# Kernel optimization log

Hardware: AMD Instinct MI355X
Metric: run time of the kernel (lower is better)

## Reference

```python
import jax, jax.numpy as jnp
import numpy as np

B, N, E = 8, 2000, 32000
LAT, STY, NF = 128, 64, 10
HEADS, HID = 4, 128
OUT = 3 + NF  # 13
EPS = 1e-5
SLOPE = 0.2


def _lin(k, fi, fo):
    return jax.random.normal(k, (fi, fo), dtype=jnp.float32) / np.sqrt(fi)


def setup_inputs() -> dict:
    key = jax.random.key(0)
    ks = jax.random.split(key, 32)
    inp = {
        'z': jax.random.normal(ks[0], (B, LAT), dtype=jnp.float32),
        'template_x': jax.random.normal(ks[1], (N, NF), dtype=jnp.float32),
        'template_edge_index': jax.random.randint(ks[2], (2, E), 0, N, dtype=jnp.int32),
        # style MLP
        'mlp_w1': _lin(ks[3], LAT, 256), 'mlp_b1': jnp.zeros((256,), jnp.float32),
        'mlp_w2': _lin(ks[4], 256, 512), 'mlp_b2': jnp.zeros((512,), jnp.float32),
        'mlp_w3': _lin(ks[5], 512, STY), 'mlp_b3': jnp.zeros((STY,), jnp.float32),
        # GAT1: in = NF + STY = 74 -> heads*HID = 512, concat
        'gat1_w': _lin(ks[6], NF + STY, HEADS * HID),
        'gat1_as': jax.random.normal(ks[7], (HEADS, HID), jnp.float32) * 0.1,
        'gat1_ad': jax.random.normal(ks[8], (HEADS, HID), jnp.float32) * 0.1,
        'gat1_b': jnp.zeros((HEADS * HID,), jnp.float32),
        'ln1_g': jnp.ones((HEADS * HID,), jnp.float32), 'ln1_b': jnp.zeros((HEADS * HID,), jnp.float32),
        # GAT2: 512 -> 512, concat
        'gat2_w': _lin(ks[9], HEADS * HID, HEADS * HID),
        'gat2_as': jax.random.normal(ks[10], (HEADS, HID), jnp.float32) * 0.1,
        'gat2_ad': jax.random.normal(ks[11], (HEADS, HID), jnp.float32) * 0.1,
        'gat2_b': jnp.zeros((HEADS * HID,), jnp.float32),
        'ln2_g': jnp.ones((HEADS * HID,), jnp.float32), 'ln2_b': jnp.zeros((HEADS * HID,), jnp.float32),
        # GAT3: 512 -> 13, 1 head, no concat
        'gat3_w': _lin(ks[12], HEADS * HID, OUT),
        'gat3_as': jax.random.normal(ks[13], (1, OUT), jnp.float32) * 0.1,
        'gat3_ad': jax.random.normal(ks[14], (1, OUT), jnp.float32) * 0.1,
        'gat3_b': jnp.zeros((OUT,), jnp.float32),
    }
    return inp


def gat_conv(x, src, dst, n_nodes, W, a_src, a_dst, bias, heads, out_ch, concat):
    # x: [NT, F_in]; per-head linear transform
    h = (x @ W).reshape(-1, heads, out_ch)              # [NT, H, C]
    als = jnp.sum(h * a_src[None], axis=-1)             # [NT, H]
    ald = jnp.sum(h * a_dst[None], axis=-1)             # [NT, H]
    logits = jax.nn.leaky_relu(als[src] + ald[dst], SLOPE)   # [E, H]
    # segment softmax over destination nodes (self-loops guarantee nonempty segments)
    mx = jax.ops.segment_max(logits, dst, num_segments=n_nodes)
    alpha = jnp.exp(logits - mx[dst])
    den = jax.ops.segment_sum(alpha, dst, num_segments=n_nodes)
    alpha = alpha / den[dst]                             # [E, H]
    msgs = h[src] * alpha[:, :, None]                    # [E, H, C]
    out = jax.ops.segment_sum(msgs, dst, num_segments=n_nodes)  # [NT, H, C]
    if concat:
        return out.reshape(n_nodes, heads * out_ch) + bias
    return out.mean(axis=1) + bias


def layer_norm(x, g, b):
    mu = jnp.mean(x, axis=-1, keepdims=True)
    var = jnp.mean((x - mu) ** 2, axis=-1, keepdims=True)
    return (x - mu) * jax.lax.rsqrt(var + EPS) * g + b


def reference(z, template_x, template_edge_index,
              mlp_w1, mlp_b1, mlp_w2, mlp_b2, mlp_w3, mlp_b3,
              gat1_w, gat1_as, gat1_ad, gat1_b, ln1_g, ln1_b,
              gat2_w, gat2_as, gat2_ad, gat2_b, ln2_g, ln2_b,
              gat3_w, gat3_as, gat3_ad, gat3_b):
    bsz = z.shape[0]
    n = template_x.shape[0]
    nt = bsz * n
    # batch the template graph: replicate nodes, offset edge indices per graph
    x = jnp.tile(template_x, (bsz, 1))                                  # [NT, NF]
    off = (jnp.arange(bsz, dtype=template_edge_index.dtype) * n)
    ei = (template_edge_index[:, None, :] + off[None, :, None]).reshape(2, -1)  # [2, B*E]
    loops = jnp.arange(nt, dtype=ei.dtype)
    src = jnp.concatenate([ei[0], loops])
    dst = jnp.concatenate([ei[1], loops])
    # style MLP
    s = jax.nn.leaky_relu(z @ mlp_w1 + mlp_b1, SLOPE)
    s = jax.nn.leaky_relu(s @ mlp_w2 + mlp_b2, SLOPE)
    s = s @ mlp_w3 + mlp_b3                                             # [B, STY]
    s_exp = jnp.repeat(s, n, axis=0)                                    # [NT, STY]
    H0 = jnp.concatenate([x, s_exp], axis=1)
    H1 = jax.nn.leaky_relu(gat_conv(H0, src, dst, nt, gat1_w, gat1_as, gat1_ad, gat1_b, HEADS, HID, True), SLOPE)
    H1n = layer_norm(H1, ln1_g, ln1_b)
    H2 = jax.nn.leaky_relu(gat_conv(H1n, src, dst, nt, gat2_w, gat2_as, gat2_ad, gat2_b, HEADS, HID, True), SLOPE)
    H2 = H2 + H1n
    H2n = layer_norm(H2, ln2_g, ln2_b)
    H_out = gat_conv(H2n, src, dst, nt, gat3_w, gat3_as, gat3_ad, gat3_b, 1, OUT, False)  # [NT, 13]
    delta_p = H_out[:, :3]
    delta_f = H_out[:, 3:]
    p_gen = x[:, :3] + delta_p
    X_gen = jnp.concatenate([p_gen, x[:, 3:] + delta_f[:, 3:]], axis=1)  # X[:, :3] overwritten by p_gen
    EF = p_gen[ei[1]] - p_gen[ei[0]]                                     # edge displacement vectors [B*E, 3]
    return X_gen, p_gen, EF
```

## Files before the change

kernel.cpp:

```cpp
#include <hip/hip_runtime.h>
#include <hip/hip_fp16.h>

constexpr int Bz = 8, Nn = 2000, Ee = 32000, NTOT = 16000;
constexpr int XG_OFF = 0, PG_OFF = 160000, EF_OFF = 208000;
#define SLOPE 0.2f
#define EPSL 1e-5f

typedef __attribute__((ext_vector_type(8))) _Float16 f16x8;
typedef __attribute__((ext_vector_type(4))) float float4v;

__device__ __forceinline__ float lrelu(float x) { return x > 0.f ? x : SLOPE * x; }

__device__ __forceinline__ unsigned short f2h(float x) {
  _Float16 hh = (_Float16)x;
  return *(unsigned short*)&hh;
}

__device__ __forceinline__ float wave_max(float v) {
  for (int o = 32; o; o >>= 1) v = fmaxf(v, __shfl_xor(v, o));
  return v;
}
__device__ __forceinline__ float wave_sum(float v) {
  for (int o = 32; o; o >>= 1) v += __shfl_xor(v, o);
  return v;
}

__global__ void hist_k(const int* __restrict__ tei, int* __restrict__ counts) {
  int j = blockIdx.x * 256 + threadIdx.x;
  if (j < Ee) atomicAdd(&counts[tei[Ee + j]], 1);
}

__global__ void scan_k(const int* __restrict__ counts, int* __restrict__ offs) {
  __shared__ int part[256];
  int t = threadIdx.x;
  int loc[8];
  int s = 0;
  for (int i = 0; i < 8; i++) {
    int idx = t * 8 + i;
    int c = (idx < Nn) ? counts[idx] : 0;
    loc[i] = s; s += c;
  }
  part[t] = s;
  __syncthreads();
  for (int o = 1; o < 256; o <<= 1) {
    int v = (t >= o) ? part[t - o] : 0;
    __syncthreads();
    part[t] += v;
    __syncthreads();
  }
  int excl = (t == 0) ? 0 : part[t - 1];
  for (int i = 0; i < 8; i++) {
    int idx = t * 8 + i;
    if (idx < Nn) offs[idx] = excl + loc[i];
  }
  if (t == 255) offs[Nn] = part[255];
}

__global__ void place_k(const int* __restrict__ tei, const int* __restrict__ offs,
                        int* __restrict__ cursor, int* __restrict__ colb) {
  int j = blockIdx.x * 256 + threadIdx.x;
  if (j < Ee) {
    int d = tei[Ee + j];
    int slot = offs[d] + atomicAdd(&cursor[d], 1);
    colb[slot] = tei[j];
  }
}

template <int K, int ACT>
__global__ __launch_bounds__(256) void lin_k(const float* __restrict__ x, const float* __restrict__ w,
                                             const float* __restrict__ bias, float* __restrict__ y,
                                             int O) {
  int gw = blockIdx.x * 4 + (threadIdx.x >> 6);
  int lane = threadIdx.x & 63;
  int bb = gw / O, o = gw - bb * O;
  float acc = 0.f;
#pragma unroll
  for (int k = lane; k < K; k += 64) acc += x[bb * K + k] * w[k * O + o];
  acc = wave_sum(acc);
  if (lane == 0) {
    if (bias) acc += bias[o];
    y[gw] = ACT ? lrelu(acc) : acc;
  }
}

__global__ __launch_bounds__(256) void w2bf_k(const float* __restrict__ W, unsigned short* __restrict__ Bt) {
  __shared__ float tile[32][33];
  int tx = threadIdx.x & 31, ty = threadIdx.x >> 5;
  int x0 = blockIdx.x * 32;
  int y0 = blockIdx.y * 32;
  for (int r = ty; r < 32; r += 8) tile[r][tx] = W[(y0 + r) * 512 + x0 + tx];
  __syncthreads();
  for (int r = ty; r < 32; r += 8) Bt[(x0 + r) * 512 + (y0 + tx)] = f2h(tile[tx][r]);
}

__global__ void w3t_k(const float* __restrict__ W, unsigned short* __restrict__ W3t) {
  for (int idx = threadIdx.x; idx < 8192; idx += 256) {
    int col = idx >> 9, k = idx & 511;
    float v = (col < 13) ? W[k * 13 + col] : 0.f;
    W3t[idx] = f2h(v);
  }
}

__global__ __launch_bounds__(256) void h1_k(const float* __restrict__ tx, const float* __restrict__ g1w,
                                            const float* __restrict__ pb,
                                            const float* __restrict__ a_s, const float* __restrict__ a_d,
                                            unsigned short* __restrict__ h1, float* __restrict__ als,
                                            float* __restrict__ ald) {
  int blk = blockIdx.x;
  int b = blk & 7, nl = blk >> 3;
  int n = b * Nn + nl;
  int head = threadIdx.x >> 6, lane = threadIdx.x & 63;
  int c = head * 128 + 2 * lane;
  float t0 = 0.f, t1 = 0.f;
#pragma unroll
  for (int k = 0; k < 10; k++) {
    float xv = tx[nl * 10 + k];
    float2 wv = *(const float2*)&g1w[k * 512 + c];
    t0 += xv * wv.x; t1 += xv * wv.y;
  }
  float2 pv = *(const float2*)&pb[b * 512 + c];
  float hx = t0 + pv.x, hy = t1 + pv.y;
  ushort2 st; st.x = f2h(hx); st.y = f2h(hy);
  *(ushort2*)&h1[(size_t)n * 512 + c] = st;
  float2 av = *(const float2*)&a_s[c];
  float2 dv = *(const float2*)&a_d[c];
  float pa = wave_sum(hx * av.x + hy * av.y);
  float pd = wave_sum(hx * dv.x + hy * dv.y);
  if (lane == 0) { als[n * 4 + head] = pa; ald[n * 4 + head] = pd; }
}

template <int RESID>
__global__ __launch_bounds__(256) void agg_k(const unsigned short* __restrict__ h,
                                             const float* __restrict__ als, const float* __restrict__ ald,
                                             const float* __restrict__ bias,
                                             const float* __restrict__ g, const float* __restrict__ beta,
                                             const unsigned short* __restrict__ resid,
                                             unsigned short* __restrict__ out,
                                             const int* __restrict__ offs, const int* __restrict__ colb) {
  int blk = blockIdx.x;
  int b = blk & 7, nl = blk >> 3;
  int n = b * Nn + nl;
  int w = threadIdx.x >> 6, lane = threadIdx.x & 63;
  int rs = offs[nl];
  int nit = offs[nl + 1] - rs + 1;
  float aldn = ald[n * 4 + w];

  __shared__ unsigned int alpha_u[4][68];
  __shared__ int sgn[64];
  __shared__ float part[4][512];
  __shared__ float invs[4];
  __shared__ float red[8];
  __shared__ float bcs[2];

  __half2 acc2[4];
#pragma unroll
  for (int j = 0; j < 4; j++) acc2[j] = __float2half2_rn(0.f);

  const unsigned short* hbase = h + lane * 8;
  int hd = lane >> 4;

  if (nit <= 64) {
    int sg = n;
    float logit = -3e38f;
    if (lane < nit) {
      sg = (lane < nit - 1) ? colb[rs + lane] + b * Nn : n;
      logit = lrelu(als[sg * 4 + w] + aldn);
      if (w == 0) sgn[lane] = sg;
    }
    float m = wave_max(logit);
    float raw = (lane < nit) ? __expf(logit - m) : 0.f;
    float den = wave_sum(raw);
    if (lane == 0) invs[w] = 1.f / den;
    __half2 a2 = __float2half2_rn(raw);
    alpha_u[w][lane] = *(unsigned int*)&a2;
    __syncthreads();
    int e = w;
    for (; e + 4 < nit; e += 8) {
      unsigned int au0 = alpha_u[hd][e];
      int sg0 = sgn[e];
      unsigned int au1 = alpha_u[hd][e + 4];
      int sg1 = sgn[e + 4];
      uint4 hv0 = *(const uint4*)(hbase + (size_t)sg0 * 512);
      uint4 hv1 = *(const uint4*)(hbase + (size_t)sg1 * 512);
      __half2 a0 = *(__half2*)&au0;
      __half2 a1 = *(__half2*)&au1;
      acc2[0] = __hfma2(a0, *(__half2*)&hv0.x, acc2[0]);
      acc2[1] = __hfma2(a0, *(__half2*)&hv0.y, acc2[1]);
      acc2[2] = __hfma2(a0, *(__half2*)&hv0.z, acc2[2]);
      acc2[3] = __hfma2(a0, *(__half2*)&hv0.w, acc2[3]);
      acc2[0] = __hfma2(a1, *(__half2*)&hv1.x, acc2[0]);
      acc2[1] = __hfma2(a1, *(__half2*)&hv1.y, acc2[1]);
      acc2[2] = __hfma2(a1, *(__half2*)&hv1.z, acc2[2]);
      acc2[3] = __hfma2(a1, *(__half2*)&hv1.w, acc2[3]);
    }
    if (e < nit) {
      unsigned int au0 = alpha_u[hd][e];
      int sg0 = sgn[e];
      uint4 hv0 = *(const uint4*)(hbase + (size_t)sg0 * 512);
      __half2 a0 = *(__half2*)&au0;
      acc2[0] = __hfma2(a0, *(__half2*)&hv0.x, acc2[0]);
      acc2[1] = __hfma2(a0, *(__half2*)&hv0.y, acc2[1]);
      acc2[2] = __hfma2(a0, *(__half2*)&hv0.z, acc2[2]);
      acc2[3] = __hfma2(a0, *(__half2*)&hv0.w, acc2[3]);
    }
  } else {
    float m = -3e38f;
    for (int i = lane; i < nit; i += 64) {
      int sg = (i < nit - 1) ? colb[rs + i] + b * Nn : n;
      m = fmaxf(m, lrelu(als[sg * 4 + w] + aldn));
    }
    m = wave_max(m);
    float den = 0.f;
    for (int base = 0; base < nit; base += 64) {
      int cnt = min(64, nit - base);
      int sg = n;
      float raw = 0.f;
      if (lane < cnt) {
        int i = base + lane;
        sg = (i < nit - 1) ? colb[rs + i] + b * Nn : n;
        raw = __expf(lrelu(als[sg * 4 + w] + aldn) - m);
        if (w == 0) sgn[lane] = sg;
      }
      den += raw;
      __half2 a2 = __float2half2_rn(raw);
      alpha_u[w][lane] = *(unsigned int*)&a2;
      __syncthreads();
      for (int e = w; e < cnt; e += 4) {
        unsigned int au = alpha_u[hd][e];
        int sge = sgn[e];
        uint4 hv = *(const uint4*)(hbase + (size_t)sge * 512);
        __half2 a2e = *(__half2*)&au;
        acc2[0] = __hfma2(a2e, *(__half2*)&hv.x, acc2[0]);
        acc2[1] = __hfma2(a2e, *(__half2*)&hv.y, acc2[1]);
        acc2[2] = __hfma2(a2e, *(__half2*)&hv.z, acc2[2]);
        acc2[3] = __hfma2(a2e, *(__half2*)&hv.w, acc2[3]);
      }
      __syncthreads();
    }
    den = wave_sum(den);
    if (lane == 0) invs[w] = 1.f / den;
  }

  float fv[8];
#pragma unroll
  for (int j = 0; j < 4; j++) {
    float2 f2 = __half22float2(acc2[j]);
    fv[2 * j] = f2.x; fv[2 * j + 1] = f2.y;
  }
  *(float4*)&part[w][lane * 8] = make_float4(fv[0], fv[1], fv[2], fv[3]);
  *(float4*)&part[w][lane * 8 + 4] = make_float4(fv[4], fv[5], fv[6], fv[7]);
  __syncthreads();

  int c = 2 * (int)threadIdx.x;
  float inv = invs[c >> 7];
  float s0 = part[0][c] + part[1][c] + part[2][c] + part[3][c];
  float s1 = part[0][c + 1] + part[1][c + 1] + part[2][c + 1] + part[3][c + 1];
  float v0 = lrelu(s0 * inv + bias[c]);
  float v1 = lrelu(s1 * inv + bias[c + 1]);
  if (RESID) {
    unsigned int rv = *(const unsigned int*)&resid[(size_t)n * 512 + c];
    __half2 rh = *(__half2*)&rv;
    float2 rf = __half22float2(rh);
    v0 += rf.x; v1 += rf.y;
  }
  float p1 = wave_sum(v0 + v1);
  float p2 = wave_sum(v0 * v0 + v1 * v1);
  if (lane == 0) { red[w] = p1; red[4 + w] = p2; }
  __syncthreads();
  if (threadIdx.x == 0) {
    float s1r = red[0] + red[1] + red[2] + red[3];
    float s2r = red[4] + red[5] + red[6] + red[7];
    float mu = s1r * (1.f / 512.f);
    float var = s2r * (1.f / 512.f) - mu * mu;
    bcs[0] = mu;
    bcs[1] = rsqrtf(var + EPSL);
  }
  __syncthreads();
  float mu = bcs[0], rstd = bcs[1];
  float o0 = (v0 - mu) * rstd * g[c] + beta[c];
  float o1 = (v1 - mu) * rstd * g[c + 1] + beta[c + 1];
  ushort2 st; st.x = f2h(o0); st.y = f2h(o1);
  *(ushort2*)&out[(size_t)n * 512 + c] = st;
}

__global__ __launch_bounds__(256) void gemm2_k(const unsigned short* __restrict__ A,
                                               const unsigned short* __restrict__ Bt,
                                               unsigned short* __restrict__ C,
                                               const float* __restrict__ As, const float* __restrict__ Ad,
                                               float* __restrict__ als2, float* __restrict__ ald2) {
  __shared__ char smem[24576];
  char* sAc = smem;
  char* sBc = smem + 8192;
  int t = threadIdx.x;
  int lane = t & 63, w = t >> 6;
  int wr = w >> 1, wc = w & 1;
  int m0 = blockIdx.y * 64, n0 = blockIdx.x * 128;
  int head = blockIdx.x;

  float4v acc[2][4];
#pragma unroll
  for (int i = 0; i < 2; i++)
#pragma unroll
    for (int j = 0; j < 4; j++) acc[i][j] = (float4v){0.f, 0.f, 0.f, 0.f};

  int sarow[2], saklin[2], sasw[2];
#pragma unroll
  for (int i = 0; i < 2; i++) {
    int slot = i * 256 + t;
    sarow[i] = slot >> 3;
    saklin[i] = (slot & 7) * 16;
    sasw[i] = sarow[i] * 128 + (saklin[i] ^ ((sarow[i] & 7) << 4));
  }
  int sbrow[4], sbklin[4], sbsw[4];
#pragma unroll
  for (int i = 0; i < 4; i++) {
    int slot = i * 256 + t;
    sbrow[i] = slot >> 3;
    sbklin[i] = (slot & 7) * 16;
    sbsw[i] = sbrow[i] * 128 + (sbklin[i] ^ ((sbrow[i] & 7) << 4));
  }

  uint4 va[2], vb[4];
#pragma unroll
  for (int i = 0; i < 2; i++)
    va[i] = *(const uint4*)((const char*)A + (size_t)(m0 + sarow[i]) * 1024 + saklin[i]);
#pragma unroll
  for (int i = 0; i < 4; i++)
    vb[i] = *(const uint4*)((const char*)Bt + (size_t)(n0 + sbrow[i]) * 1024 + sbklin[i]);

  int r_a = wr * 32 + (lane & 15);
  int r_b = wc * 64 + (lane & 15);
  int kbb = (lane >> 4) * 16;
  int sw_a = (r_a & 7) << 4;
  int sw_b = (r_b & 7) << 4;

  for (int k0 = 0; k0 < 512; k0 += 64) {
    if (k0) __syncthreads();
#pragma unroll
    for (int i = 0; i < 2; i++) *(uint4*)(sAc + sasw[i]) = va[i];
#pragma unroll
    for (int i = 0; i < 4; i++) *(uint4*)(sBc + sbsw[i]) = vb[i];
    __syncthreads();
    if (k0 + 64 < 512) {
#pragma unroll
      for (int i = 0; i < 2; i++)
        va[i] = *(const uint4*)((const char*)A + (size_t)(m0 + sarow[i]) * 1024 + (k0 + 64) * 2 + saklin[i]);
#pragma unroll
      for (int i = 0; i < 4; i++)
        vb[i] = *(const uint4*)((const char*)Bt + (size_t)(n0 + sbrow[i]) * 1024 + (k0 + 64) * 2 + sbklin[i]);
    }
#pragma unroll
    for (int ksub = 0; ksub < 2; ksub++) {
      f16x8 af[2], bg[4];
#pragma unroll
      for (int m = 0; m < 2; m++)
        af[m] = *(const f16x8*)(sAc + (r_a + m * 16) * 128 + ((ksub * 64 + kbb) ^ sw_a));
#pragma unroll
      for (int nn = 0; nn < 4; nn++)
        bg[nn] = *(const f16x8*)(sBc + (r_b + nn * 16) * 128 + ((ksub * 64 + kbb) ^ sw_b));
#pragma unroll
      for (int m = 0; m < 2; m++)
#pragma unroll
        for (int nn = 0; nn < 4; nn++)
          acc[m][nn] = __builtin_amdgcn_mfma_f32_16x16x32_f16(af[m], bg[nn], acc[m][nn], 0, 0, 0);
    }
  }

  __syncthreads();
  unsigned short* sC = (unsigned short*)smem;
  int rbase = wr * 32 + (lane >> 4) * 4;
  int cbase = wc * 64 + (lane & 15);
#pragma unroll
  for (int m = 0; m < 2; m++)
#pragma unroll
    for (int nn = 0; nn < 4; nn++)
#pragma unroll
      for (int r = 0; r < 4; r++)
        sC[(rbase + m * 16 + r) * 136 + cbase + nn * 16] = f2h(acc[m][nn][r]);
  __syncthreads();
#pragma unroll
  for (int p = 0; p < 4; p++) {
    int row = p * 16 + (t >> 4);
    int co = (t & 15) * 8;
    uint4 v = *(const uint4*)&sC[row * 136 + co];
    *(uint4*)&C[(size_t)(m0 + row) * 512 + n0 + co] = v;
  }

  __syncthreads();
  float* sRed = (float*)smem;
  int cidx0 = wc * 64 + (lane & 15);
  float asv[4], adv[4];
#pragma unroll
  for (int nn = 0; nn < 4; nn++) {
    asv[nn] = As[head * 128 + cidx0 + nn * 16];
    adv[nn] = Ad[head * 128 + cidx0 + nn * 16];
  }
#pragma unroll
  for (int m = 0; m < 2; m++) {
#pragma unroll
    for (int r = 0; r < 4; r++) {
      float pa = 0.f, pd = 0.f;
#pragma unroll
      for (int nn = 0; nn < 4; nn++) { pa += acc[m][nn][r] * asv[nn]; pd += acc[m][nn][r] * adv[nn]; }
      for (int o = 1; o < 16; o <<= 1) { pa += __shfl_xor(pa, o); pd += __shfl_xor(pd, o); }
      if ((lane & 15) == 0) {
        int rblk = wr * 32 + (lane >> 4) * 4 + m * 16 + r;
        sRed[rblk * 2 + wc] = pa;
        sRed[128 + rblk * 2 + wc] = pd;
      }
    }
  }
  __syncthreads();
  if (t < 64) {
    als2[(m0 + t) * 4 + head] = sRed[t * 2] + sRed[t * 2 + 1];
  } else if (t < 128) {
    int r2 = t - 64;
    ald2[(m0 + r2) * 4 + head] = sRed[128 + r2 * 2] + sRed[128 + r2 * 2 + 1];
  }
}

__global__ __launch_bounds__(256) void gemm3_k(const unsigned short* __restrict__ H,
                                               const unsigned short* __restrict__ W3t,
                                               const float* __restrict__ as3, const float* __restrict__ ad3,
                                               float* __restrict__ h3, float* __restrict__ als3,
                                               float* __restrict__ ald3) {
  int w = threadIdx.x >> 6, l = threadIdx.x & 63;
  int m0 = blockIdx.x * 64 + w * 16;
  int r16 = l & 15, g4 = l >> 4;
  float4v acc = (float4v){0.f, 0.f, 0.f, 0.f};
  const unsigned short* ha = H + (size_t)(m0 + r16) * 512 + g4 * 8;
  const unsigned short* wb = W3t + (size_t)r16 * 512 + g4 * 8;
#pragma unroll
  for (int kk = 0; kk < 16; kk++) {
    f16x8 a = *(const f16x8*)(ha + kk * 32);
    f16x8 bfr = *(const f16x8*)(wb + kk * 32);
    acc = __builtin_amdgcn_mfma_f32_16x16x32_f16(a, bfr, acc, 0, 0, 0);
  }
  int col = r16;
  float asv = (col < 13) ? as3[col] : 0.f;
  float adv = (col < 13) ? ad3[col] : 0.f;
#pragma unroll
  for (int r = 0; r < 4; r++) {
    float v = acc[r];
    int row = m0 + g4 * 4 + r;
    if (col < 13) h3[row * 13 + col] = v;
    float sa = v * asv, sd = v * adv;
    for (int o = 1; o < 16; o <<= 1) { sa += __shfl_xor(sa, o); sd += __shfl_xor(sd, o); }
    if (col == 0) { als3[row] = sa; ald3[row] = sd; }
  }
}

__global__ __launch_bounds__(64) void agg3_k(const float* __restrict__ h3, const float* __restrict__ als3,
                                             const float* __restrict__ ald3, const float* __restrict__ b3,
                                             const float* __restrict__ tx, const int* __restrict__ offs,
                                             const int* __restrict__ colb, float* __restrict__ dout) {
  int blk = blockIdx.x, lane = threadIdx.x;
  int b = blk & 7, nl = blk >> 3;
  int n = b * Nn + nl;
  int rs = offs[nl], deg = offs[nl + 1] - rs;
  float aldn = ald3[n];
  float sl = lrelu(als3[n] + aldn);
  float a = 0.f, inv;
  if (deg <= 64) {
    int sgl = 0; float logit = -1e30f;
    if (lane < deg) { sgl = colb[rs + lane] + b * Nn; logit = lrelu(als3[sgl] + aldn); }
    float m = wave_max(fmaxf(logit, sl));
    float raw = (lane < deg) ? __expf(logit - m) : 0.f;
    float es = __expf(sl - m);
    inv = 1.f / (wave_sum(raw) + es);
    if (lane < 13) a = es * h3[n * 13 + lane];
    for (int e = 0; e < deg; e++) {
      float w = __shfl(raw, e);
      int sg = __shfl(sgl, e);
      if (lane < 13) a += w * h3[sg * 13 + lane];
    }
  } else {
    float m = sl;
    for (int e = lane; e < deg; e += 64) {
      int sg = colb[rs + e] + b * Nn;
      m = fmaxf(m, lrelu(als3[sg] + aldn));
    }
    m = wave_max(m);
    float es = __expf(sl - m);
    float den = (lane == 0) ? es : 0.f;
    if (lane < 13) a = es * h3[n * 13 + lane];
    for (int base = 0; base < deg; base += 64) {
      int cnt = min(64, deg - base);
      int sgl = 0; float raw = 0.f;
      if (lane < cnt) {
        sgl = colb[rs + base + lane] + b * Nn;
        raw = __expf(lrelu(als3[sgl] + aldn) - m);
      }
      den += raw;
      for (int e = 0; e < cnt; e++) {
        float w = __shfl(raw, e);
        int sg = __shfl(sgl, e);
        if (lane < 13) a += w * h3[sg * 13 + lane];
      }
    }
    inv = 1.f / wave_sum(den);
  }
  a *= inv;
  float hv = a + ((lane < 13) ? b3[lane] : 0.f);
  float txv = (lane < 10) ? tx[nl * 10 + lane] : 0.f;
  float pv = txv + hv;
  if (lane < 3) dout[PG_OFF + n * 3 + lane] = pv;
  float up = __shfl(hv, lane + 3);
  float xg = (lane < 3) ? pv : (txv + up);
  if (lane < 10) dout[XG_OFF + n * 10 + lane] = xg;
}

__global__ void ef_k(const int* __restrict__ tei, float* __restrict__ dout) {
  int e = blockIdx.x * 256 + threadIdx.x;
  int b = e / Ee, j = e - b * Ee;
  int sg = tei[j] + b * Nn;
  int dg = tei[Ee + j] + b * Nn;
  const float* pg = dout + PG_OFF;
  dout[EF_OFF + e * 3 + 0] = pg[dg * 3 + 0] - pg[sg * 3 + 0];
  dout[EF_OFF + e * 3 + 1] = pg[dg * 3 + 1] - pg[sg * 3 + 1];
  dout[EF_OFF + e * 3 + 2] = pg[dg * 3 + 2] - pg[sg * 3 + 2];
}

extern "C" void kernel_launch(void* const* d_in, const int* in_sizes, int n_in,
                              void* d_out, int out_size, void* d_ws, size_t ws_size,
                              hipStream_t stream) {
  const float* z = (const float*)d_in[0];
  const float* tx = (const float*)d_in[1];
  const int* tei = (const int*)d_in[2];
  const float* w1 = (const float*)d_in[3];
  const float* b1 = (const float*)d_in[4];
  const float* w2 = (const float*)d_in[5];
  const float* b2 = (const float*)d_in[6];
  const float* w3 = (const float*)d_in[7];
  const float* b3 = (const float*)d_in[8];
  const float* g1w = (const float*)d_in[9];
  const float* g1as = (const float*)d_in[10];
  const float* g1ad = (const float*)d_in[11];
  const float* g1b = (const float*)d_in[12];
  const float* ln1g = (const float*)d_in[13];
  const float* ln1b = (const float*)d_in[14];
  const float* g2w = (const float*)d_in[15];
  const float* g2as = (const float*)d_in[16];
  const float* g2ad = (const float*)d_in[17];
  const float* g2b = (const float*)d_in[18];
  const float* ln2g = (const float*)d_in[19];
  const float* ln2b = (const float*)d_in[20];
  const float* g3w = (const float*)d_in[21];
  const float* g3as = (const float*)d_in[22];
  const float* g3ad = (const float*)d_in[23];
  const float* g3b = (const float*)d_in[24];
  float* out = (float*)d_out;

  float* F = (float*)d_ws;
  float* pb_ = F + 0;
  float* l1_ = F + 8192;
  float* l2_ = F + 16384;
  float* s_ = F + 24576;
  float* als1 = F + 100000;
  float* ald1 = F + 164000;
  float* als2 = F + 228000;
  float* ald2 = F + 292000;
  float* als3 = F + 356000;
  float* ald3 = F + 372000;
  float* h3_ = F + 388000;
  unsigned short* U = (unsigned short*)(F + 600000);
  unsigned short* hA = U;
  unsigned short* hB = U + 8192000;
  unsigned short* Bt = U + 16384000;
  unsigned short* W3t = U + 16646144;
  int* I = (int*)(F + 10000000);
  int* counts = I;
  int* cursor = I + 2000;
  int* offs = I + 4000;
  int* colb = I + 6001;

  hipMemsetAsync(counts, 0, 4000 * sizeof(int), stream);
  hist_k<<<125, 256, 0, stream>>>(tei, counts);
  scan_k<<<1, 256, 0, stream>>>(counts, offs);
  place_k<<<125, 256, 0, stream>>>(tei, offs, cursor, colb);

  w2bf_k<<<dim3(16, 16), 256, 0, stream>>>(g2w, Bt);
  w3t_k<<<1, 256, 0, stream>>>(g3w, W3t);

  lin_k<128, 1><<<512, 256, 0, stream>>>(z, w1, b1, l1_, 256);
  lin_k<256, 1><<<1024, 256, 0, stream>>>(l1_, w2, b2, l2_, 512);
  lin_k<512, 0><<<128, 256, 0, stream>>>(l2_, w3, b3, s_, 64);
  lin_k<64, 0><<<1024, 256, 0, stream>>>(s_, g1w + 10 * 512, nullptr, pb_, 512);

  h1_k<<<NTOT, 256, 0, stream>>>(tx, g1w, pb_, g1as, g1ad, hA, als1, ald1);
  agg_k<0><<<NTOT, 256, 0, stream>>>(hA, als1, ald1, g1b, ln1g, ln1b, nullptr, hB, offs, colb);

  gemm2_k<<<dim3(4, 250), 256, 0, stream>>>(hB, Bt, hA, g2as, g2ad, als2, ald2);
  agg_k<1><<<NTOT, 256, 0, stream>>>(hA, als2, ald2, g2b, ln2g, ln2b, hB, hB, offs, colb);

  gemm3_k<<<250, 256, 0, stream>>>(hB, W3t, g3as, g3ad, h3_, als3, ald3);
  agg3_k<<<NTOT, 64, 0, stream>>>(h3_, als3, ald3, g3b, tx, offs, colb, out);
  ef_k<<<1000, 256, 0, stream>>>(tei, out);
}
```

Measured before the change: 230.8 us.

## Widen gemm2 tile to full 512 columns per block with 8 waves

The layer-2 GEMM now has each block compute a 64x512 output tile with 512 threads, so one block covers all four heads for its rows instead of one head per block. The A tile is loaded once per row block rather than four times. Attention logits are written straight from registers because each wave owns a whole head, which removes the shared-memory reduction pass. The cost is 250 blocks instead of 1000, a 72KB LDS footprint and 64 accumulator vectors per thread, all of which reduce occupancy and CU coverage.

```diff
diff --git a/kernel.cpp b/kernel.cpp
--- a/kernel.cpp
+++ b/kernel.cpp
@@ -283,139 +283,118 @@
   *(ushort2*)&out[(size_t)n * 512 + c] = st;
 }
 
-__global__ __launch_bounds__(256) void gemm2_k(const unsigned short* __restrict__ A,
+__global__ __launch_bounds__(512) void gemm2_k(const unsigned short* __restrict__ A,
                                                const unsigned short* __restrict__ Bt,
                                                unsigned short* __restrict__ C,
                                                const float* __restrict__ As, const float* __restrict__ Ad,
                                                float* __restrict__ als2, float* __restrict__ ald2) {
-  __shared__ char smem[24576];
+  __shared__ char smem[73728];
   char* sAc = smem;
   char* sBc = smem + 8192;
   int t = threadIdx.x;
   int lane = t & 63, w = t >> 6;
-  int wr = w >> 1, wc = w & 1;
-  int m0 = blockIdx.y * 64, n0 = blockIdx.x * 128;
-  int head = blockIdx.x;
-
-  float4v acc[2][4];
+  int wm = w >> 2, wn = w & 3;
+  int m0 = blockIdx.x * 64;
+
+  float4v acc[2][8];
 #pragma unroll
   for (int i = 0; i < 2; i++)
 #pragma unroll
-    for (int j = 0; j < 4; j++) acc[i][j] = (float4v){0.f, 0.f, 0.f, 0.f};
-
-  int sarow[2], saklin[2], sasw[2];
-#pragma unroll
-  for (int i = 0; i < 2; i++) {
-    int slot = i * 256 + t;
-    sarow[i] = slot >> 3;
-    saklin[i] = (slot & 7) * 16;
-    sasw[i] = sarow[i] * 128 + (saklin[i] ^ ((sarow[i] & 7) << 4));
-  }
-  int sbrow[4], sbklin[4], sbsw[4];
-#pragma unroll
-  for (int i = 0; i < 4; i++) {
-    int slot = i * 256 + t;
-    sbrow[i] = slot >> 3;
-    sbklin[i] = (slot & 7) * 16;
-    sbsw[i] = sbrow[i] * 128 + (sbklin[i] ^ ((sbrow[i] & 7) << 4));
-  }
-
-  uint4 va[2], vb[4];
-#pragma unroll
-  for (int i = 0; i < 2; i++)
-    va[i] = *(const uint4*)((const char*)A + (size_t)(m0 + sarow[i]) * 1024 + saklin[i]);
-#pragma unroll
-  for (int i = 0; i < 4; i++)
-    vb[i] = *(const uint4*)((const char*)Bt + (size_t)(n0 + sbrow[i]) * 1024 + sbklin[i]);
-
-  int r_a = wr * 32 + (lane & 15);
-  int r_b = wc * 64 + (lane & 15);
+    for (int j = 0; j < 8; j++) acc[i][j] = (float4v){0.f, 0.f, 0.f, 0.f};
+
+  int arow = t >> 3, aklin = (t & 7) * 16;
+  int asw = arow * 128 + (aklin ^ ((arow & 7) << 4));
+  int brow[8], bklin[8], bsw[8];
+#pragma unroll
+  for (int i = 0; i < 8; i++) {
+    int slot = i * 512 + t;
+    brow[i] = slot >> 3;
+    bklin[i] = (slot & 7) * 16;
+    bsw[i] = brow[i] * 128 + (bklin[i] ^ ((brow[i] & 7) << 4));
+  }
+
+  uint4 va = *(const uint4*)((const char*)A + (size_t)(m0 + arow) * 1024 + aklin);
+  uint4 vb[8];
+#pragma unroll
+  for (int i = 0; i < 8; i++)
+    vb[i] = *(const uint4*)((const char*)Bt + (size_t)brow[i] * 1024 + bklin[i]);
+
+  int r_a = wm * 32 + (lane & 15);
+  int r_b = wn * 128 + (lane & 15);
   int kbb = (lane >> 4) * 16;
-  int sw_a = (r_a & 7) << 4;
-  int sw_b = (r_b & 7) << 4;
+  int sw = ((lane & 15) & 7) << 4;
 
   for (int k0 = 0; k0 < 512; k0 += 64) {
     if (k0) __syncthreads();
-#pragma unroll
-    for (int i = 0; i < 2; i++) *(uint4*)(sAc + sasw[i]) = va[i];
-#pragma unroll
-    for (int i = 0; i < 4; i++) *(uint4*)(sBc + sbsw[i]) = vb[i];
+    *(uint4*)(sAc + asw) = va;
+#pragma unroll
+    for (int i = 0; i < 8; i++) *(uint4*)(sBc + bsw[i]) = vb[i];
     __syncthreads();
     if (k0 + 64 < 512) {
-#pragma unroll
-      for (int i = 0; i < 2; i++)
-        va[i] = *(const uint4*)((const char*)A + (size_t)(m0 + sarow[i]) * 1024 + (k0 + 64) * 2 + saklin[i]);
-#pragma unroll
-      for (int i = 0; i < 4; i++)
-        vb[i] = *(const uint4*)((const char*)Bt + (size_t)(n0 + sbrow[i]) * 1024 + (k0 + 64) * 2 + sbklin[i]);
+      va = *(const uint4*)((const char*)A + (size_t)(m0 + arow) * 1024 + (k0 + 64) * 2 + aklin);
+#pragma unroll
+      for (int i = 0; i < 8; i++)
+        vb[i] = *(const uint4*)((const char*)Bt + (size_t)brow[i] * 1024 + (k0 + 64) * 2 + bklin[i]);
     }
 #pragma unroll
     for (int ksub = 0; ksub < 2; ksub++) {
-      f16x8 af[2], bg[4];
+      f16x8 af[2], bg[8];
 #pragma unroll
       for (int m = 0; m < 2; m++)
-        af[m] = *(const f16x8*)(sAc + (r_a + m * 16) * 128 + ((ksub * 64 + kbb) ^ sw_a));
-#pragma unroll
-      for (int nn = 0; nn < 4; nn++)
-        bg[nn] = *(const f16x8*)(sBc + (r_b + nn * 16) * 128 + ((ksub * 64 + kbb) ^ sw_b));
+        af[m] = *(const f16x8*)(sAc + (r_a + m * 16) * 128 + ((ksub * 64 + kbb) ^ sw));
+#pragma unroll
+      for (int nn = 0; nn < 8; nn++)
+        bg[nn] = *(const f16x8*)(sBc + (r_b + nn * 16) * 128 + ((ksub * 64 + kbb) ^ sw));
 #pragma unroll
       for (int m = 0; m < 2; m++)
 #pragma unroll
-        for (int nn = 0; nn < 4; nn++)
+        for (int nn = 0; nn < 8; nn++)
           acc[m][nn] = __builtin_amdgcn_mfma_f32_16x16x32_f16(af[m], bg[nn], acc[m][nn], 0, 0, 0);
     }
   }
 
+  {
+    float asv[8], adv[8];
+#pragma unroll
+    for (int nn = 0; nn < 8; nn++) {
+      asv[nn] = As[wn * 128 + nn * 16 + (lane & 15)];
+      adv[nn] = Ad[wn * 128 + nn * 16 + (lane & 15)];
+    }
+#pragma unroll
+    for (int m = 0; m < 2; m++) {
+#pragma unroll
+      for (int r = 0; r < 4; r++) {
+        float pa = 0.f, pd = 0.f;
+#pragma unroll
+        for (int nn = 0; nn < 8; nn++) { pa += acc[m][nn][r] * asv[nn]; pd += acc[m][nn][r] * adv[nn]; }
+        for (int o = 1; o < 16; o <<= 1) { pa += __shfl_xor(pa, o); pd += __shfl_xor(pd, o); }
+        if ((lane & 15) == 0) {
+          int row = m0 + wm * 32 + (lane >> 4) * 4 + m * 16 + r;
+          als2[row * 4 + wn] = pa;
+          ald2[row * 4 + wn] = pd;
+        }
+      }
+    }
+  }
+
   __syncthreads();
   unsigned short* sC = (unsigned short*)smem;
-  int rbase = wr * 32 + (lane >> 4) * 4;
-  int cbase = wc * 64 + (lane & 15);
+  int rbase = wm * 32 + (lane >> 4) * 4;
+  int cbase = wn * 128 + (lane & 15);
 #pragma unroll
   for (int m = 0; m < 2; m++)
 #pragma unroll
-    for (int nn = 0; nn < 4; nn++)
+    for (int nn = 0; nn < 8; nn++)
 #pragma unroll
       for (int r = 0; r < 4; r++)
-        sC[(rbase + m * 16 + r) * 136 + cbase + nn * 16] = f2h(acc[m][nn][r]);
-  __syncthreads();
-#pragma unroll
-  for (int p = 0; p < 4; p++) {
-    int row = p * 16 + (t >> 4);
-    int co = (t & 15) * 8;
-    uint4 v = *(const uint4*)&sC[row * 136 + co];
-    *(uint4*)&C[(size_t)(m0 + row) * 512 + n0 + co] = v;
-  }
-
-  __syncthreads();
-  float* sRed = (float*)smem;
-  int cidx0 = wc * 64 + (lane & 15);
-  float asv[4], adv[4];
-#pragma unroll
-  for (int nn = 0; nn < 4; nn++) {
-    asv[nn] = As[head * 128 + cidx0 + nn * 16];
-    adv[nn] = Ad[head * 128 + cidx0 + nn * 16];
-  }
-#pragma unroll
-  for (int m = 0; m < 2; m++) {
-#pragma unroll
-    for (int r = 0; r < 4; r++) {
-      float pa = 0.f, pd = 0.f;
-#pragma unroll
-      for (int nn = 0; nn < 4; nn++) { pa += acc[m][nn][r] * asv[nn]; pd += acc[m][nn][r] * adv[nn]; }
-      for (int o = 1; o < 16; o <<= 1) { pa += __shfl_xor(pa, o); pd += __shfl_xor(pd, o); }
-      if ((lane & 15) == 0) {
-        int rblk = wr * 32 + (lane >> 4) * 4 + m * 16 + r;
-        sRed[rblk * 2 + wc] = pa;
-        sRed[128 + rblk * 2 + wc] = pd;
-      }
-    }
-  }
-  __syncthreads();
-  if (t < 64) {
-    als2[(m0 + t) * 4 + head] = sRed[t * 2] + sRed[t * 2 + 1];
-  } else if (t < 128) {
-    int r2 = t - 64;
-    ald2[(m0 + r2) * 4 + head] = sRed[128 + r2 * 2] + sRed[128 + r2 * 2 + 1];
+        sC[(rbase + m * 16 + r) * 520 + cbase + nn * 16] = f2h(acc[m][nn][r]);
+  __syncthreads();
+#pragma unroll
+  for (int p = 0; p < 8; p++) {
+    int row = p * 8 + (t >> 6);
+    int co = (t & 63) * 8;
+    uint4 v = *(const uint4*)&sC[row * 520 + co];
+    *(uint4*)&C[(size_t)(m0 + row) * 512 + co] = v;
   }
 }
 
@@ -590,7 +569,7 @@
   h1_k<<<NTOT, 256, 0, stream>>>(tx, g1w, pb_, g1as, g1ad, hA, als1, ald1);
   agg_k<0><<<NTOT, 256, 0, stream>>>(hA, als1, ald1, g1b, ln1g, ln1b, nullptr, hB, offs, colb);
 
-  gemm2_k<<<dim3(4, 250), 256, 0, stream>>>(hB, Bt, hA, g2as, g2ad, als2, ald2);
+  gemm2_k<<<250, 512, 0, stream>>>(hB, Bt, hA, g2as, g2ad, als2, ald2);
   agg_k<1><<<NTOT, 256, 0, stream>>>(hA, als2, ald2, g2b, ln2g, ln2b, hB, hB, offs, colb);
 
   gemm3_k<<<250, 256, 0, stream>>>(hB, W3t, g3as, g3ad, h3_, als3, ald3);
```

Measured after the change: 216.5 us. 6.2% less time.
